# Kernel optimization log

Hardware: AMD Instinct MI355X
Metric: run time of the kernel (lower is better)

## Reference

```python
import jax, jax.numpy as jnp
import numpy as np

B, T, S0 = 8, 4, 4096
D_MODEL, H, D, R, RANK = 2048, 16, 128, 64, 512
C = D - R  # content dim = 64


def _rope(x, positions):
    # x: [B, H, T, R]; rotate-half style RoPE as in the torch module
    half = x.shape[-1] // 2
    inv_freq = 1.0 / (10000.0 ** (jnp.arange(half, dtype=jnp.float32) / half))
    freqs = positions.astype(jnp.float32)[:, None] * inv_freq[None, :]  # [T, half]
    cos = jnp.cos(freqs)[None, None].astype(x.dtype)
    sin = jnp.sin(freqs)[None, None].astype(x.dtype)
    x1, x2 = x[..., :half], x[..., half:]
    return jnp.concatenate([x1 * cos - x2 * sin, x1 * sin + x2 * cos], axis=-1)


def setup_inputs() -> dict:
    key = jax.random.key(0)
    ks = jax.random.split(key, 9)
    s = 0.02
    return {
        "x": jax.random.normal(ks[0], (B, T, D_MODEL), jnp.float32),
        "cache_c_kv": jax.random.normal(ks[1], (B, S0, RANK), jnp.float32),
        "cache_k_rope": jax.random.normal(ks[2], (B, S0, H, R), jnp.float32),
        "w_q": jax.random.normal(ks[3], (D_MODEL, H * C), jnp.float32) * s,
        "w_q_rope": jax.random.normal(ks[4], (D_MODEL, H * R), jnp.float32) * s,
        "w_kv_down": jax.random.normal(ks[5], (D_MODEL, RANK), jnp.float32) * s,
        "w_kv_up": jax.random.normal(ks[6], (RANK, H * D), jnp.float32) * s,
        "w_k_rope": jax.random.normal(ks[7], (D_MODEL, H * R), jnp.float32) * s,
        "w_out": jax.random.normal(ks[8], (H * D, D_MODEL), jnp.float32) * s,
    }


def reference(x, cache_c_kv, cache_k_rope, w_q, w_q_rope, w_kv_down, w_kv_up, w_k_rope, w_out):
    cache_len = cache_c_kv.shape[1]
    positions = jnp.arange(cache_len, cache_len + T)

    # queries
    q_content = (x @ w_q).reshape(B, T, H, C).transpose(0, 2, 1, 3)        # [B,H,T,C]
    q_rope = (x @ w_q_rope).reshape(B, T, H, R).transpose(0, 2, 1, 3)      # [B,H,T,R]
    q_rope = _rope(q_rope, positions)
    q = jnp.concatenate([q_content, q_rope], axis=-1)                       # [B,H,T,D]

    # new compressed kv + rope keys, append to cache
    c_kv_new = x @ w_kv_down                                                # [B,T,RANK]
    k_rope_new = (x @ w_k_rope).reshape(B, T, H, R).transpose(0, 2, 1, 3)
    k_rope_new = _rope(k_rope_new, positions).transpose(0, 2, 1, 3)         # [B,T,H,R]
    c_kv = jnp.concatenate([cache_c_kv, c_kv_new], axis=1)                  # [B,S,RANK]
    k_rope = jnp.concatenate([cache_k_rope, k_rope_new], axis=1)            # [B,S,H,R]

    # decompress full cache every step (the expensive MLA pattern)
    S = c_kv.shape[1]
    kv = (c_kv @ w_kv_up).reshape(B, S, H, D)                               # [B,S,H,D]
    k_content = kv[..., :C].transpose(0, 2, 1, 3)                           # [B,H,S,C]
    v = kv.transpose(0, 2, 1, 3)                                            # [B,H,S,D]
    k = jnp.concatenate([k_content, k_rope.transpose(0, 2, 1, 3)], axis=-1) # [B,H,S,D]

    # kv_cache present => is_prefill False => no causal mask (faithful to source)
    scale = 1.0 / jnp.sqrt(jnp.asarray(D, dtype=q.dtype))
    scores = jnp.einsum('bhtd,bhsd->bhts', q, k) * scale
    attn = jax.nn.softmax(scores, axis=-1)
    out = jnp.einsum('bhts,bhsd->bhtd', attn, v)                            # [B,H,T,D]
    out = out.transpose(0, 2, 1, 3).reshape(B, T, H * D)
    return out @ w_out                                                       # [B,T,D_MODEL]
```

## Files before the change

kernel.cpp:

```cpp
#include <hip/hip_runtime.h>
#include <hip/hip_fp16.h>
#include <cmath>

#define BB 8
#define TT 4
#define HH 16
#define DDIM 128
#define RRDIM 64
#define CCDIM 64
#define RANKC 512
#define DMODEL 2048
#define S0C 4096
#define NQ 64
#define HD 2048
#define NACT 3584
#define NSC 65
#define NG 17
#define SPAD 4160
#define SCALE_ATT 0.08838834764831845f

typedef __attribute__((ext_vector_type(8))) short bf16x8;
typedef __attribute__((ext_vector_type(4))) float f32x4;
typedef unsigned short ushortT;

#define AIDX(row, kk) ((row)*132 + (((row)>>2)<<2) + (kk))

static __device__ __forceinline__ unsigned short f2bf(float x) {
  unsigned u = __float_as_uint(x);
  u += 0x7FFFu + ((u >> 16) & 1u);
  return (unsigned short)(u >> 16);
}
static __device__ __forceinline__ unsigned pk2(float a, float b) {
  return (unsigned)f2bf(a) | ((unsigned)f2bf(b) << 16);
}

__global__ __launch_bounds__(256) void k_front(const float* __restrict__ A,
                                               const float* __restrict__ w0,
                                               const float* __restrict__ w1,
                                               const float* __restrict__ w2,
                                               const float* __restrict__ w3,
                                               const float* __restrict__ cckv,
                                               float* __restrict__ part,
                                               ushortT* __restrict__ ckvB,
                                               ushortT* __restrict__ ckvT) {
  __shared__ float shf[4352];
  const int tid = threadIdx.x;
  const int bx = blockIdx.x;
  if (bx < 448) {
    const int cb = bx % 28;
    const int k0 = (bx / 28) * 128;
    const float* W; int N, lc0, off;
    if (cb < 8)       { W = w0; N = 1024; lc0 = cb * 128;        off = 0; }
    else if (cb < 16) { W = w1; N = 1024; lc0 = (cb - 8) * 128;  off = 1024; }
    else if (cb < 20) { W = w2; N = 512;  lc0 = (cb - 16) * 128; off = 2048; }
    else              { W = w3; N = 1024; lc0 = (cb - 20) * 128; off = 2560; }
    {
      const int row = tid >> 3;
      const int kseg = (tid & 7) * 16;
      const float4* s4 = reinterpret_cast<const float4*>(A + (size_t)row * DMODEL + k0 + kseg);
      float4 v0 = s4[0], v1 = s4[1], v2 = s4[2], v3 = s4[3];
      *reinterpret_cast<float4*>(&shf[AIDX(row, kseg)])      = v0;
      *reinterpret_cast<float4*>(&shf[AIDX(row, kseg + 4)])  = v1;
      *reinterpret_cast<float4*>(&shf[AIDX(row, kseg + 8)])  = v2;
      *reinterpret_cast<float4*>(&shf[AIDX(row, kseg + 12)]) = v3;
    }
    __syncthreads();
    const int cg = tid & 31;
    const int rg = tid >> 5;
    float acc[4][4];
    #pragma unroll
    for (int r = 0; r < 4; ++r)
      #pragma unroll
      for (int c = 0; c < 4; ++c) acc[r][c] = 0.f;
    #pragma unroll 4
    for (int kk = 0; kk < 128; ++kk) {
      const float4 w4 = *reinterpret_cast<const float4*>(W + (size_t)(k0 + kk) * N + lc0 + cg * 4);
      const float wv[4] = {w4.x, w4.y, w4.z, w4.w};
      #pragma unroll
      for (int r = 0; r < 4; ++r) {
        const float av = shf[AIDX(rg * 4 + r, kk)];
        #pragma unroll
        for (int c = 0; c < 4; ++c) acc[r][c] = fmaf(av, wv[c], acc[r][c]);
      }
    }
    #pragma unroll
    for (int r = 0; r < 4; ++r) {
      float4 o = make_float4(acc[r][0], acc[r][1], acc[r][2], acc[r][3]);
      *reinterpret_cast<float4*>(part + ((size_t)(bx / 28) * 32 + rg * 4 + r) * NACT + off + lc0 + cg * 4) = o;
    }
  } else if (bx < 960) {
    ushortT* tlds = reinterpret_cast<ushortT*>(shf);
    const int idx = bx - 448;
    const int b = idx >> 6, c = idx & 63;
    const float* src = cckv + ((size_t)b * S0C + c * 64) * RANKC;
    ushortT* dstB = ckvB + ((size_t)(b * NSC + c) * 64) * RANKC;
    ushortT* dstT = ckvT + ((size_t)(b * NSC + c) * RANKC) * 64;
    const int s = tid >> 2, rq = tid & 3;
    const int rloc = tid >> 1, shalf = (tid & 1) * 32;
    for (int slab = 0; slab < 4; ++slab) {
      const int r0 = slab * 128;
      #pragma unroll
      for (int i = 0; i < 8; ++i) {
        const float4 v = *reinterpret_cast<const float4*>(src + (size_t)s * RANKC + r0 + rq * 32 + i * 4);
        const uint2 pk = make_uint2(pk2(v.x, v.y), pk2(v.z, v.w));
        *reinterpret_cast<uint2*>(&tlds[s * 136 + rq * 32 + i * 4]) = pk;
        *reinterpret_cast<uint2*>(&dstB[(size_t)s * RANKC + r0 + rq * 32 + i * 4]) = pk;
      }
      __syncthreads();
      unsigned pkv[16];
      #pragma unroll
      for (int k = 0; k < 16; ++k) {
        const unsigned t0 = tlds[(shalf + 2 * k)     * 136 + rloc];
        const unsigned t1 = tlds[(shalf + 2 * k + 1) * 136 + rloc];
        pkv[k] = t0 | (t1 << 16);
      }
      uint4* d = reinterpret_cast<uint4*>(dstT + ((size_t)(r0 + rloc)) * 64 + shalf);
      d[0] = make_uint4(pkv[0], pkv[1], pkv[2], pkv[3]);
      d[1] = make_uint4(pkv[4], pkv[5], pkv[6], pkv[7]);
      d[2] = make_uint4(pkv[8], pkv[9], pkv[10], pkv[11]);
      d[3] = make_uint4(pkv[12], pkv[13], pkv[14], pkv[15]);
      __syncthreads();
    }
  } else if (bx < 968) {
    const int b = bx - 960;
    uint4* p = reinterpret_cast<uint4*>(ckvB + ((size_t)(b * NSC + 64) * 64) * RANKC);
    const uint4 z = make_uint4(0, 0, 0, 0);
    for (int i = tid; i < 4096; i += 256) p[i] = z;
  } else {
    const int b = bx - 968;
    uint4* p = reinterpret_cast<uint4*>(ckvT + ((size_t)(b * NSC + 64) * RANKC) * 64);
    const uint4 z = make_uint4(0, 0, 0, 0);
    for (int i = tid; i < 4096; i += 256) p[i] = z;
  }
}

__global__ __launch_bounds__(256) void k_proj(const float* __restrict__ A,
                                              const float* __restrict__ W,
                                              float* __restrict__ part,
                                              int N, int NTOT, int coloff) {
  __shared__ float a_lds[4352];
  const int tid = threadIdx.x;
  const int c0 = blockIdx.x * 128;
  const int k0 = blockIdx.y * 128;
  {
    const int row = tid >> 3;
    const int kseg = (tid & 7) * 16;
    const float4* s4 = reinterpret_cast<const float4*>(A + (size_t)row * DMODEL + k0 + kseg);
    float4 v0 = s4[0], v1 = s4[1], v2 = s4[2], v3 = s4[3];
    *reinterpret_cast<float4*>(&a_lds[AIDX(row, kseg)])      = v0;
    *reinterpret_cast<float4*>(&a_lds[AIDX(row, kseg + 4)])  = v1;
    *reinterpret_cast<float4*>(&a_lds[AIDX(row, kseg + 8)])  = v2;
    *reinterpret_cast<float4*>(&a_lds[AIDX(row, kseg + 12)]) = v3;
  }
  __syncthreads();
  const int cg = tid & 31;
  const int rg = tid >> 5;
  float acc[4][4];
  #pragma unroll
  for (int r = 0; r < 4; ++r)
    #pragma unroll
    for (int c = 0; c < 4; ++c) acc[r][c] = 0.f;
  #pragma unroll 4
  for (int kk = 0; kk < 128; ++kk) {
    const float4 w4 = *reinterpret_cast<const float4*>(W + (size_t)(k0 + kk) * N + c0 + cg * 4);
    const float wv[4] = {w4.x, w4.y, w4.z, w4.w};
    #pragma unroll
    for (int r = 0; r < 4; ++r) {
      const float av = a_lds[AIDX(rg * 4 + r, kk)];
      #pragma unroll
      for (int c = 0; c < 4; ++c) acc[r][c] = fmaf(av, wv[c], acc[r][c]);
    }
  }
  #pragma unroll
  for (int r = 0; r < 4; ++r) {
    float4 o = make_float4(acc[r][0], acc[r][1], acc[r][2], acc[r][3]);
    *reinterpret_cast<float4*>(part + ((size_t)blockIdx.y * 32 + rg * 4 + r) * NTOT + coloff + c0 + cg * 4) = o;
  }
}

__global__ __launch_bounds__(256) void k_reduce(const float* __restrict__ part,
                                                float* __restrict__ out, int total, int nsplit) {
  int g = blockIdx.x * 256 + threadIdx.x;
  if (g >= total) return;
  float s = 0.f;
  #pragma unroll 4
  for (int c = 0; c < nsplit; ++c) s += part[(size_t)c * total + g];
  out[g] = s;
}

__global__ __launch_bounds__(256) void k_qlatrope(const float* __restrict__ act,
                                                  const float* __restrict__ wup,
                                                  ushortT* __restrict__ qlat,
                                                  float* __restrict__ qrope,
                                                  float* __restrict__ krn,
                                                  ushortT* __restrict__ ckvB,
                                                  ushortT* __restrict__ ckvT) {
  __shared__ float wt[64 * 132];
  __shared__ float a_s[32 * 68];
  const int tid = threadIdx.x;
  const int bx = blockIdx.x;
  if (bx < 64) {
    const int h = bx & 15;
    const int r0 = (bx >> 4) * 128;
    {
      const int r = tid >> 1;
      const int cseg = (tid & 1) * 32;
      const float* src = wup + (size_t)(r0 + r) * HD + h * DDIM + cseg;
      #pragma unroll
      for (int u = 0; u < 8; ++u) {
        const float4 v = *reinterpret_cast<const float4*>(src + u * 4);
        wt[(cseg + u * 4 + 0) * 132 + r] = v.x;
        wt[(cseg + u * 4 + 1) * 132 + r] = v.y;
        wt[(cseg + u * 4 + 2) * 132 + r] = v.z;
        wt[(cseg + u * 4 + 3) * 132 + r] = v.w;
      }
    }
    {
      const int bt = tid >> 3;
      const int cseg = (tid & 7) * 8;
      const float4* s4 = reinterpret_cast<const float4*>(act + (size_t)bt * NACT + h * CCDIM + cseg);
      float4 v0 = s4[0], v1 = s4[1];
      *reinterpret_cast<float4*>(&a_s[bt * 68 + cseg])     = v0;
      *reinterpret_cast<float4*>(&a_s[bt * 68 + cseg + 4]) = v1;
    }
    __syncthreads();
    const int r = tid & 127;
    const int bth = tid >> 7;
    float acc[16];
    #pragma unroll
    for (int i = 0; i < 16; ++i) acc[i] = 0.f;
    #pragma unroll 8
    for (int c = 0; c < 64; ++c) {
      const float wv = wt[c * 132 + r];
      #pragma unroll
      for (int i = 0; i < 16; ++i)
        acc[i] = fmaf(a_s[(bth * 16 + i) * 68 + c], wv, acc[i]);
    }
    #pragma unroll
    for (int i = 0; i < 16; ++i) {
      const int bt = bth * 16 + i;
      const int b = bt >> 2, t = bt & 3;
      qlat[((size_t)(b * NQ) + h * TT + t) * RANKC + r0 + r] = f2bf(acc[i]);
    }
    return;
  }
  int g = (bx - 64) * 256 + tid;
  if (g < BB * TT * HH * 32) {
    const int hj = g & 31;
    const int h = (g >> 5) & 15;
    const int t = (g >> 9) & 3;
    const int b = g >> 11;
    const float* arow = act + (size_t)(b * TT + t) * NACT + 1024 + h * RRDIM;
    const float x1 = arow[hj], x2 = arow[hj + 32];
    const double fr = (double)(S0C + t) * pow(10000.0, -(double)hj / 32.0);
    const float cs = (float)cos(fr), sn = (float)sin(fr);
    const int qi = h * TT + t;
    qrope[((size_t)b * NQ + qi) * RRDIM + hj]      = x1 * cs - x2 * sn;
    qrope[((size_t)b * NQ + qi) * RRDIM + hj + 32] = x1 * sn + x2 * cs;
    return;
  }
  g -= BB * TT * HH * 32;
  if (g < BB * TT * HH * 32) {
    const int hj = g & 31;
    const int h = (g >> 5) & 15;
    const int t = (g >> 9) & 3;
    const int b = g >> 11;
    const float* arow = act + (size_t)(b * TT + t) * NACT + 2560 + h * RRDIM;
    const float x1 = arow[hj], x2 = arow[hj + 32];
    const double fr = (double)(S0C + t) * pow(10000.0, -(double)hj / 32.0);
    const float cs = (float)cos(fr), sn = (float)sin(fr);
    krn[((size_t)(b * TT + t) * HH + h) * RRDIM + hj]      = x1 * cs - x2 * sn;
    krn[((size_t)(b * TT + t) * HH + h) * RRDIM + hj + 32] = x1 * sn + x2 * cs;
    return;
  }
  g -= BB * TT * HH * 32;
  if (g < BB * TT * RANKC) {
    const int r = g & 511;
    const int bt = g >> 9;
    const int b = bt >> 2, t = bt & 3;
    const ushortT bv = f2bf(act[(size_t)bt * NACT + 2048 + r]);
    ckvB[(((size_t)(b * NSC + 64) * 64) + t) * RANKC + r] = bv;
    ckvT[(((size_t)(b * NSC + 64) * RANKC) + r) * 64 + t] = bv;
  }
}

__global__ __launch_bounds__(256) void k_rscore(const float* __restrict__ cache_kr,
                                                const float* __restrict__ krn,
                                                const float* __restrict__ qrope,
                                                __half* __restrict__ rs) {
  const int bh = blockIdx.x;
  const int b = bh >> 4, h = bh & 15;
  const int tid = threadIdx.x;
  const int ql = tid & 3;
  float4 qf[4][4];
  const float* qrb = qrope + ((size_t)b * NQ + h * TT) * RRDIM;
  #pragma unroll
  for (int t = 0; t < 4; ++t)
    #pragma unroll
    for (int u = 0; u < 4; ++u)
      qf[t][u] = *reinterpret_cast<const float4*>(qrb + t * RRDIM + ql * 16 + u * 4);
  const int s0 = blockIdx.y * 512;
  #pragma unroll 1
  for (int pass = 0; pass < 8; ++pass) {
    const int s = s0 + pass * 64 + (tid >> 2);
    if (s < 4100) {
      const float* krow = (s < S0C)
        ? cache_kr + (((size_t)b * S0C + s) * HH + h) * RRDIM
        : krn + (((size_t)b * TT + (s - S0C)) * HH + h) * RRDIM;
      float p[4] = {0.f, 0.f, 0.f, 0.f};
      #pragma unroll
      for (int u = 0; u < 4; ++u) {
        const float4 kv = *reinterpret_cast<const float4*>(krow + ql * 16 + u * 4);
        #pragma unroll
        for (int t = 0; t < 4; ++t) {
          p[t] += kv.x * qf[t][u].x + kv.y * qf[t][u].y
                + kv.z * qf[t][u].z + kv.w * qf[t][u].w;
        }
      }
      #pragma unroll
      for (int t = 0; t < 4; ++t) {
        p[t] += __shfl_xor(p[t], 1, 4);
        p[t] += __shfl_xor(p[t], 2, 4);
      }
      rs[((size_t)bh * 4 + ql) * SPAD + s] = __float2half(p[ql] * SCALE_ATT);
    }
  }
}

__global__ __launch_bounds__(128) void k_score(
    const ushortT* __restrict__ ckvB, const ushortT* __restrict__ qlat,
    const __half* __restrict__ rs, float* __restrict__ ml,
    ushortT* __restrict__ Pg) {
  __shared__ ushortT PL[2][16 * 72];
  const int tid = threadIdx.x;
  const int wv = tid >> 6;
  const int lane = tid & 63;
  const int lm = lane & 15, lg = lane >> 4;
  const int b = blockIdx.x, chunk = blockIdx.y;
  const int qbase = blockIdx.z * 32 + wv * 16;
  const int scnt = (chunk < 64) ? 64 : TT;

  const ushortT* qrow = qlat + ((size_t)b * NQ + qbase + lm) * RANKC + lg * 8;
  bf16x8 qa[16];
  #pragma unroll
  for (int ks = 0; ks < 16; ++ks)
    qa[ks] = *reinterpret_cast<const bf16x8*>(qrow + ks * 32);

  const ushortT* bbase = ckvB + ((size_t)(b * NSC + chunk) * 64) * RANKC;
  f32x4 acc[4];
  #pragma unroll
  for (int st = 0; st < 4; ++st) acc[st] = (f32x4){0.f, 0.f, 0.f, 0.f};
  #pragma unroll
  for (int ks = 0; ks < 16; ++ks) {
    #pragma unroll
    for (int st = 0; st < 4; ++st) {
      const bf16x8 bf = *reinterpret_cast<const bf16x8*>(
          bbase + (size_t)(st * 16 + lm) * RANKC + ks * 32 + lg * 8);
      acc[st] = __builtin_amdgcn_mfma_f32_16x16x32_bf16(qa[ks], bf, acc[st], 0, 0, 0);
    }
  }

  #pragma unroll
  for (int reg = 0; reg < 4; ++reg) {
    const int qi = qbase + lg * 4 + reg;
    const __half* rp = rs + (((size_t)(b * HH) + (qi >> 2)) * TT + (qi & 3)) * SPAD + chunk * 64;
    float vvv[4];
    float mx = -1e30f;
    #pragma unroll
    for (int st = 0; st < 4; ++st) {
      const int sl = st * 16 + lm;
      const float val = (sl < scnt)
          ? fmaf(acc[st][reg], SCALE_ATT, __half2float(rp[sl]))
          : -1e30f;
      vvv[st] = val;
      mx = fmaxf(mx, val);
    }
    #pragma unroll
    for (int off = 1; off < 16; off <<= 1) mx = fmaxf(mx, __shfl_xor(mx, off, 16));
    float sum = 0.f;
    #pragma unroll
    for (int st = 0; st < 4; ++st) {
      const float p = __expf(vvv[st] - mx);
      vvv[st] = p;
      sum += p;
    }
    #pragma unroll
    for (int off = 1; off < 16; off <<= 1) sum += __shfl_xor(sum, off, 16);
    #pragma unroll
    for (int st = 0; st < 4; ++st)
      PL[wv][(lg * 4 + reg) * 72 + st * 16 + lm] = f2bf(vvv[st]);
    if (lm == 0) {
      const size_t mb = (((size_t)b * NSC + chunk) * NQ + qi) * 2;
      ml[mb] = mx; ml[mb + 1] = sum;
    }
  }
  __syncthreads();
  {
    const int row = lane >> 2, seg = (lane & 3) * 16;
    const uint4* sp = reinterpret_cast<const uint4*>(&PL[wv][row * 72 + seg]);
    uint4* dp = reinterpret_cast<uint4*>(
        Pg + ((size_t)(b * NSC + chunk) * NQ + qbase + row) * 64 + seg);
    dp[0] = sp[0]; dp[1] = sp[1];
  }
}

__global__ __launch_bounds__(128) void k_pv(
    const ushortT* __restrict__ ckvT, const ushortT* __restrict__ Pg,
    const float* __restrict__ ml, float* __restrict__ olat,
    float* __restrict__ mlg) {
  const int tid = threadIdx.x;
  const int wv = tid >> 6;
  const int lane = tid & 63;
  const int lm = lane & 15, lg = lane >> 4;
  const int b = blockIdx.x, g = blockIdx.y;
  const int rg = blockIdx.z >> 1, qh = blockIdx.z & 1;
  const int qbase = qh * 32 + wv * 16;
  const int nc = (g < 16) ? 4 : 1;
  const int c0 = (g < 16) ? g * 4 : 64;

  float m_cl = -1e30f, l_cl = 0.f;
  if (lg < nc) {
    const size_t mb = (((size_t)b * NSC + c0 + lg) * NQ + qbase + lm) * 2;
    m_cl = ml[mb]; l_cl = ml[mb + 1];
  }
  float mg = fmaxf(m_cl, __shfl_xor(m_cl, 16));
  mg = fmaxf(mg, __shfl_xor(mg, 32));
  const float wgt = (lg < nc) ? __expf(m_cl - mg) : 0.f;
  float la = l_cl * wgt;
  la += __shfl_xor(la, 16);
  la += __shfl_xor(la, 32);
  if (rg == 0 && lg == 0) {
    const size_t gb = (((size_t)b * NG + g) * NQ + qbase + lm) * 2;
    mlg[gb] = mg; mlg[gb + 1] = la;
  }
  float wf[4][4];
  #pragma unroll
  for (int c = 0; c < 4; ++c)
    #pragma unroll
    for (int reg = 0; reg < 4; ++reg)
      wf[c][reg] = __shfl(wgt, c * 16 + lg * 4 + reg);

  f32x4 OACC[8];
  #pragma unroll
  for (int nt = 0; nt < 8; ++nt) OACC[nt] = (f32x4){0.f, 0.f, 0.f, 0.f};

  for (int c = 0; c < nc; ++c) {
    const ushortT* pb = Pg + ((size_t)(b * NSC + c0 + c) * NQ + qbase + lm) * 64 + lg * 8;
    const bf16x8 pa0 = *reinterpret_cast<const bf16x8*>(pb);
    const bf16x8 pa1 = *reinterpret_cast<const bf16x8*>(pb + 32);
    const ushortT* vb = ckvT + (((size_t)(b * NSC + c0 + c) * RANKC) + rg * 128 + lm) * 64 + lg * 8;
    f32x4 a2[8];
    #pragma unroll
    for (int nt = 0; nt < 8; ++nt) a2[nt] = (f32x4){0.f, 0.f, 0.f, 0.f};
    #pragma unroll
    for (int nt = 0; nt < 8; ++nt) {
      const bf16x8 b0 = *reinterpret_cast<const bf16x8*>(vb + (size_t)nt * 16 * 64);
      const bf16x8 b1 = *reinterpret_cast<const bf16x8*>(vb + (size_t)nt * 16 * 64 + 32);
      a2[nt] = __builtin_amdgcn_mfma_f32_16x16x32_bf16(pa0, b0, a2[nt], 0, 0, 0);
      a2[nt] = __builtin_amdgcn_mfma_f32_16x16x32_bf16(pa1, b1, a2[nt], 0, 0, 0);
    }
    const f32x4 wv4 = {wf[c][0], wf[c][1], wf[c][2], wf[c][3]};
    #pragma unroll
    for (int nt = 0; nt < 8; ++nt) OACC[nt] += wv4 * a2[nt];
  }

  const size_t obase = ((size_t)(b * NG + g) * NQ) * RANKC;
  #pragma unroll
  for (int nt = 0; nt < 8; ++nt)
    #pragma unroll
    for (int reg = 0; reg < 4; ++reg)
      olat[obase + (size_t)(qbase + lg * 4 + reg) * RANKC + rg * 128 + nt * 16 + lm] = OACC[nt][reg];
}

__global__ __launch_bounds__(512) void k_combF(const float* __restrict__ mlg,
                                               const float* __restrict__ olat,
                                               const float* __restrict__ wup,
                                               float* __restrict__ ohead) {
  __shared__ float wrow[4][20];
  __shared__ float att_lds[4][516];
  const int h = blockIdx.x, b = blockIdx.y;
  const int tid = threadIdx.x;
  const int wave = tid >> 6;
  const int i = wave >> 1;
  const int rhalf = wave & 1;
  const int rl = tid & 63;
  const int qi = h * TT + i;
  float m1 = -1e30f, l1 = 0.f;
  if (rl < NG) {
    const size_t base = (((size_t)b * NG + rl) * NQ + qi) * 2;
    m1 = mlg[base]; l1 = mlg[base + 1];
  }
  float M = m1;
  #pragma unroll
  for (int off = 1; off < 64; off <<= 1) M = fmaxf(M, __shfl_xor(M, off));
  float L = (rl < NG) ? l1 * __expf(m1 - M) : 0.f;
  #pragma unroll
  for (int off = 1; off < 64; off <<= 1) L += __shfl_xor(L, off);
  const float invL = 1.0f / L;
  if (rl < NG) wrow[i][rl] = __expf(m1 - M) * invL;
  __syncthreads();
  const int r0 = rhalf * 256 + rl * 4;
  float o0 = 0.f, o1 = 0.f, o2 = 0.f, o3 = 0.f;
  for (int c = 0; c < NG; ++c) {
    const float w = wrow[i][c];
    const float4 v = *reinterpret_cast<const float4*>(
        olat + (((size_t)b * NG + c) * NQ + qi) * RANKC + r0);
    o0 = fmaf(v.x, w, o0); o1 = fmaf(v.y, w, o1);
    o2 = fmaf(v.z, w, o2); o3 = fmaf(v.w, w, o3);
  }
  *reinterpret_cast<float4*>(&att_lds[i][r0]) = make_float4(o0, o1, o2, o3);
  __syncthreads();
  const int col = tid & 127;
  const int t = tid >> 7;
  float acc = 0.f;
  #pragma unroll 8
  for (int r = 0; r < RANKC; ++r)
    acc = fmaf(att_lds[t][r], wup[(size_t)r * HD + h * DDIM + col], acc);
  ohead[(size_t)(b * TT + t) * HD + h * DDIM + col] = acc;
}

extern "C" void kernel_launch(void* const* d_in, const int* in_sizes, int n_in,
                              void* d_out, int out_size, void* d_ws, size_t ws_size,
                              hipStream_t stream) {
  const float* x     = (const float*)d_in[0];
  const float* cckv  = (const float*)d_in[1];
  const float* ckr   = (const float*)d_in[2];
  const float* w_q   = (const float*)d_in[3];
  const float* w_qr  = (const float*)d_in[4];
  const float* w_kvd = (const float*)d_in[5];
  const float* w_kvu = (const float*)d_in[6];
  const float* w_kr  = (const float*)d_in[7];
  const float* w_out = (const float*)d_in[8];
  float* out = (float*)d_out;
  float* ws = (float*)d_ws;

  size_t off = 0;
  float* act      = ws + off; off += 32ull * NACT;
  ushortT* qlat   = (ushortT*)(ws + off); off += 131072;
  float* qrope    = ws + off; off += 32768;
  float* krn      = ws + off; off += 32768;
  float* mlb      = ws + off; off += (size_t)BB * NSC * NQ * 2;
  float* mlgb     = ws + off; off += (size_t)BB * NG * NQ * 2;
  float* ohead    = ws + off; off += 65536;
  __half* rsb     = (__half*)(ws + off); off += 1064960;
  ushortT* ckvB   = (ushortT*)(ws + off); off += 8519680;
  ushortT* ckvT   = (ushortT*)(ws + off); off += 8519680;
  ushortT* Pgb    = (ushortT*)(ws + off); off += 1064960;
  float* regB  = ws + off;
  float* part0 = regB;
  float* olat  = regB;
  float* part3 = regB;

  k_front<<<dim3(976), 256, 0, stream>>>(x, w_q, w_qr, w_kvd, w_kr, cckv, part0, ckvB, ckvT);
  k_reduce<<<dim3(448), 256, 0, stream>>>(part0, act, 32 * NACT, 16);
  k_qlatrope<<<dim3(256), 256, 0, stream>>>(act, w_kvu, qlat, qrope, krn, ckvB, ckvT);
  k_rscore<<<dim3(128, 9), 256, 0, stream>>>(ckr, krn, qrope, rsb);

  k_score<<<dim3(BB, NSC, 2), 128, 0, stream>>>(ckvB, qlat, rsb, mlb, Pgb);
  k_pv<<<dim3(BB, NG, 8), 128, 0, stream>>>(ckvT, Pgb, mlb, olat, mlgb);

  k_combF<<<dim3(16, 8), 512, 0, stream>>>(mlgb, olat, w_kvu, ohead);
  k_proj<<<dim3(16, 16), 256, 0, stream>>>(ohead, w_out, part3, 2048, 2048, 0);
  k_reduce<<<dim3(256), 256, 0, stream>>>(part3, out, 32 * HD, 16);
}
```

Baseline: 213.0 us.

## Fuse reduce, q-latent, rope-score stages and drop bf16 row-major cache copy

Three kernels (the split-K reduce, the q-latent/rope kernel and the rope-score kernel) are merged into a single k_mid kernel that sums the split-K partials directly where each stage needs them. The row-major bf16 copy of the compressed cache is removed. k_score now reads the fp32 cache and converts it to bf16 on the fly, with new tokens held in a small fp32 buffer. The score and PV kernels use 256-thread blocks covering all 64 queries, which halves their grid sizes. This cuts launches and a large bf16 write, but the score kernel reads twice as many bytes per cache element and repeats the partial sums per block.

```diff
diff --git a/kernel.cpp b/kernel.cpp
--- a/kernel.cpp
+++ b/kernel.cpp
@@ -33,6 +33,11 @@
 static __device__ __forceinline__ unsigned pk2(float a, float b) {
   return (unsigned)f2bf(a) | ((unsigned)f2bf(b) << 16);
 }
+static __device__ __forceinline__ bf16x8 cvt8(const float4 a, const float4 b) {
+  union { uint4 u; bf16x8 h; } r;
+  r.u = make_uint4(pk2(a.x, a.y), pk2(a.z, a.w), pk2(b.x, b.y), pk2(b.z, b.w));
+  return r.h;
+}
 
 __global__ __launch_bounds__(256) void k_front(const float* __restrict__ A,
                                                const float* __restrict__ w0,
@@ -41,8 +46,8 @@
                                                const float* __restrict__ w3,
                                                const float* __restrict__ cckv,
                                                float* __restrict__ part,
-                                               ushortT* __restrict__ ckvB,
-                                               ushortT* __restrict__ ckvT) {
+                                               ushortT* __restrict__ ckvT,
+                                               float* __restrict__ ckvn) {
   __shared__ float shf[4352];
   const int tid = threadIdx.x;
   const int bx = blockIdx.x;
@@ -93,7 +98,6 @@
     const int idx = bx - 448;
     const int b = idx >> 6, c = idx & 63;
     const float* src = cckv + ((size_t)b * S0C + c * 64) * RANKC;
-    ushortT* dstB = ckvB + ((size_t)(b * NSC + c) * 64) * RANKC;
     ushortT* dstT = ckvT + ((size_t)(b * NSC + c) * RANKC) * 64;
     const int s = tid >> 2, rq = tid & 3;
     const int rloc = tid >> 1, shalf = (tid & 1) * 32;
@@ -102,9 +106,8 @@
       #pragma unroll
       for (int i = 0; i < 8; ++i) {
         const float4 v = *reinterpret_cast<const float4*>(src + (size_t)s * RANKC + r0 + rq * 32 + i * 4);
-        const uint2 pk = make_uint2(pk2(v.x, v.y), pk2(v.z, v.w));
-        *reinterpret_cast<uint2*>(&tlds[s * 136 + rq * 32 + i * 4]) = pk;
-        *reinterpret_cast<uint2*>(&dstB[(size_t)s * RANKC + r0 + rq * 32 + i * 4]) = pk;
+        *reinterpret_cast<uint2*>(&tlds[s * 136 + rq * 32 + i * 4]) =
+            make_uint2(pk2(v.x, v.y), pk2(v.z, v.w));
       }
       __syncthreads();
       unsigned pkv[16];
@@ -121,17 +124,362 @@
       d[3] = make_uint4(pkv[12], pkv[13], pkv[14], pkv[15]);
       __syncthreads();
     }
-  } else if (bx < 968) {
+  } else {
     const int b = bx - 960;
-    uint4* p = reinterpret_cast<uint4*>(ckvB + ((size_t)(b * NSC + 64) * 64) * RANKC);
     const uint4 z = make_uint4(0, 0, 0, 0);
+    uint4* p = reinterpret_cast<uint4*>(ckvT + ((size_t)(b * NSC + 64) * RANKC) * 64);
     for (int i = tid; i < 4096; i += 256) p[i] = z;
+    uint4* q = reinterpret_cast<uint4*>(ckvn + ((size_t)b * 64 + 4) * RANKC);
+    for (int i = tid; i < 7680; i += 256) q[i] = z;
+  }
+}
+
+__global__ __launch_bounds__(256) void k_mid(const float* __restrict__ part0,
+                                             const float* __restrict__ cache_kr,
+                                             const float* __restrict__ wup,
+                                             ushortT* __restrict__ qlat,
+                                             float* __restrict__ ckvn,
+                                             ushortT* __restrict__ ckvT,
+                                             __half* __restrict__ rs) {
+  __shared__ float smid[10880];
+  const int tid = threadIdx.x;
+  const int bx = blockIdx.x;
+  if (bx < 1152) {
+    const int bh = bx / 9, sy = bx % 9;
+    const int b = bh >> 4, h = bh & 15;
+    float* raw_q = smid;
+    float* raw_k = smid + 256;
+    float* qr_l  = smid + 512;
+    float* kr_l  = smid + 768;
+    {
+      const int t = tid >> 6, j = tid & 63;
+      const size_t rowoff = (size_t)(b * TT + t) * NACT;
+      float sq = 0.f, sk = 0.f;
+      #pragma unroll 4
+      for (int ks = 0; ks < 16; ++ks) {
+        const float* pp = part0 + (size_t)ks * (32 * NACT) + rowoff;
+        sq += pp[1024 + h * 64 + j];
+        sk += pp[2560 + h * 64 + j];
+      }
+      raw_q[t * 64 + j] = sq;
+      raw_k[t * 64 + j] = sk;
+    }
+    __syncthreads();
+    {
+      const int t = tid >> 6, j = tid & 63;
+      const int j2 = j & 31;
+      const double inv = pow(10000.0, -(double)j2 / 32.0);
+      const double fr = (double)(S0C + t) * inv;
+      const float cs = (float)cos(fr), sn = (float)sin(fr);
+      const float qa = raw_q[t * 64 + j], qp = raw_q[t * 64 + (j ^ 32)];
+      const float ka = raw_k[t * 64 + j], kp = raw_k[t * 64 + (j ^ 32)];
+      float qv, kv;
+      if (j < 32) { qv = qa * cs - qp * sn; kv = ka * cs - kp * sn; }
+      else        { qv = qp * sn + qa * cs; kv = kp * sn + ka * cs; }
+      qr_l[t * 64 + j] = qv * SCALE_ATT;
+      kr_l[t * 64 + j] = kv;
+    }
+    __syncthreads();
+    const int ql = tid & 3;
+    float4 qf[4][4];
+    #pragma unroll
+    for (int t = 0; t < 4; ++t)
+      #pragma unroll
+      for (int u = 0; u < 4; ++u)
+        qf[t][u] = *reinterpret_cast<const float4*>(&qr_l[t * 64 + ql * 16 + u * 4]);
+    const int s0 = sy * 512;
+    #pragma unroll 1
+    for (int pass = 0; pass < 8; ++pass) {
+      const int s = s0 + pass * 64 + (tid >> 2);
+      if (s < 4100) {
+        float p[4] = {0.f, 0.f, 0.f, 0.f};
+        if (s < S0C) {
+          const float* krow = cache_kr + (((size_t)b * S0C + s) * HH + h) * RRDIM;
+          #pragma unroll
+          for (int u = 0; u < 4; ++u) {
+            const float4 kv = *reinterpret_cast<const float4*>(krow + ql * 16 + u * 4);
+            #pragma unroll
+            for (int t = 0; t < 4; ++t)
+              p[t] += kv.x * qf[t][u].x + kv.y * qf[t][u].y
+                    + kv.z * qf[t][u].z + kv.w * qf[t][u].w;
+          }
+        } else {
+          const float* krow = &kr_l[(s - S0C) * 64];
+          #pragma unroll
+          for (int u = 0; u < 4; ++u) {
+            const float4 kv = *reinterpret_cast<const float4*>(krow + ql * 16 + u * 4);
+            #pragma unroll
+            for (int t = 0; t < 4; ++t)
+              p[t] += kv.x * qf[t][u].x + kv.y * qf[t][u].y
+                    + kv.z * qf[t][u].z + kv.w * qf[t][u].w;
+          }
+        }
+        #pragma unroll
+        for (int t = 0; t < 4; ++t) {
+          p[t] += __shfl_xor(p[t], 1, 4);
+          p[t] += __shfl_xor(p[t], 2, 4);
+        }
+        rs[((size_t)bh * 4 + ql) * SPAD + s] = __float2half(p[ql]);
+      }
+    }
+  } else if (bx < 1216) {
+    const int lx = bx - 1152;
+    const int h = lx & 15;
+    const int r0 = (lx >> 4) * 128;
+    float* wt  = smid;
+    float* a_s = smid + 8448;
+    {
+      const int r = tid >> 1;
+      const int cseg = (tid & 1) * 32;
+      const float* src = wup + (size_t)(r0 + r) * HD + h * DDIM + cseg;
+      #pragma unroll
+      for (int u = 0; u < 8; ++u) {
+        const float4 v = *reinterpret_cast<const float4*>(src + u * 4);
+        wt[(cseg + u * 4 + 0) * 132 + r] = v.x;
+        wt[(cseg + u * 4 + 1) * 132 + r] = v.y;
+        wt[(cseg + u * 4 + 2) * 132 + r] = v.z;
+        wt[(cseg + u * 4 + 3) * 132 + r] = v.w;
+      }
+    }
+    {
+      const int bt = tid >> 3;
+      const int c8 = (tid & 7) * 8;
+      float v[8] = {0.f,0.f,0.f,0.f,0.f,0.f,0.f,0.f};
+      #pragma unroll 4
+      for (int ks = 0; ks < 16; ++ks) {
+        const float4* pp = reinterpret_cast<const float4*>(
+            part0 + (size_t)ks * (32 * NACT) + (size_t)bt * NACT + h * CCDIM + c8);
+        const float4 x0 = pp[0], x1 = pp[1];
+        v[0]+=x0.x; v[1]+=x0.y; v[2]+=x0.z; v[3]+=x0.w;
+        v[4]+=x1.x; v[5]+=x1.y; v[6]+=x1.z; v[7]+=x1.w;
+      }
+      #pragma unroll
+      for (int u = 0; u < 8; ++u) a_s[bt * 68 + c8 + u] = v[u];
+    }
+    __syncthreads();
+    const int r = tid & 127;
+    const int bth = tid >> 7;
+    float acc[16];
+    #pragma unroll
+    for (int i = 0; i < 16; ++i) acc[i] = 0.f;
+    #pragma unroll 8
+    for (int c = 0; c < 64; ++c) {
+      const float wv = wt[c * 132 + r];
+      #pragma unroll
+      for (int i = 0; i < 16; ++i)
+        acc[i] = fmaf(a_s[(bth * 16 + i) * 68 + c], wv, acc[i]);
+    }
+    #pragma unroll
+    for (int i = 0; i < 16; ++i) {
+      const int bt = bth * 16 + i;
+      const int b = bt >> 2, t = bt & 3;
+      qlat[((size_t)(b * NQ) + h * TT + t) * RANKC + r0 + r] = f2bf(acc[i]);
+    }
   } else {
-    const int b = bx - 968;
-    uint4* p = reinterpret_cast<uint4*>(ckvT + ((size_t)(b * NSC + 64) * RANKC) * 64);
-    const uint4 z = make_uint4(0, 0, 0, 0);
-    for (int i = tid; i < 4096; i += 256) p[i] = z;
-  }
+    const int g = (bx - 1216) * 256 + tid;
+    const int r = g & 511;
+    const int bt = g >> 9;
+    const int b = bt >> 2, t = bt & 3;
+    float s = 0.f;
+    #pragma unroll 4
+    for (int ks = 0; ks < 16; ++ks)
+      s += part0[(size_t)ks * (32 * NACT) + (size_t)bt * NACT + 2048 + r];
+    ckvn[((size_t)b * 64 + t) * RANKC + r] = s;
+    ckvT[(((size_t)(b * NSC + 64) * RANKC) + r) * 64 + t] = f2bf(s);
+  }
+}
+
+__global__ __launch_bounds__(256) void k_score(
+    const float* __restrict__ cckv, const float* __restrict__ ckvn,
+    const ushortT* __restrict__ qlat, const __half* __restrict__ rs,
+    float* __restrict__ ml, ushortT* __restrict__ Pg) {
+  __shared__ ushortT PL[64 * 72];
+  const int tid = threadIdx.x;
+  const int wv = tid >> 6;
+  const int lane = tid & 63;
+  const int lm = lane & 15, lg = lane >> 4;
+  const int b = blockIdx.x, chunk = blockIdx.y;
+  const int qbase = wv * 16;
+  const int scnt = (chunk < 64) ? 64 : TT;
+  const float* bsrc = (chunk < 64)
+      ? cckv + ((size_t)b * S0C + (size_t)chunk * 64) * RANKC
+      : ckvn + (size_t)b * 64 * RANKC;
+
+  const ushortT* qrow = qlat + ((size_t)b * NQ + qbase + lm) * RANKC + lg * 8;
+  bf16x8 qa[16];
+  #pragma unroll
+  for (int ks = 0; ks < 16; ++ks)
+    qa[ks] = *reinterpret_cast<const bf16x8*>(qrow + ks * 32);
+
+  f32x4 acc[4];
+  #pragma unroll
+  for (int st = 0; st < 4; ++st) acc[st] = (f32x4){0.f, 0.f, 0.f, 0.f};
+  #pragma unroll
+  for (int ks = 0; ks < 16; ++ks) {
+    #pragma unroll
+    for (int st = 0; st < 4; ++st) {
+      const float4* bp = reinterpret_cast<const float4*>(
+          bsrc + (size_t)(st * 16 + lm) * RANKC + ks * 32 + lg * 8);
+      acc[st] = __builtin_amdgcn_mfma_f32_16x16x32_bf16(qa[ks], cvt8(bp[0], bp[1]), acc[st], 0, 0, 0);
+    }
+  }
+
+  #pragma unroll
+  for (int reg = 0; reg < 4; ++reg) {
+    const int qi = qbase + lg * 4 + reg;
+    const __half* rp = rs + (((size_t)(b * HH) + (qi >> 2)) * TT + (qi & 3)) * SPAD + chunk * 64;
+    float vvv[4];
+    float mx = -1e30f;
+    #pragma unroll
+    for (int st = 0; st < 4; ++st) {
+      const int sl = st * 16 + lm;
+      const float val = (sl < scnt)
+          ? fmaf(acc[st][reg], SCALE_ATT, __half2float(rp[sl]))
+          : -1e30f;
+      vvv[st] = val;
+      mx = fmaxf(mx, val);
+    }
+    #pragma unroll
+    for (int off = 1; off < 16; off <<= 1) mx = fmaxf(mx, __shfl_xor(mx, off, 16));
+    float sum = 0.f;
+    #pragma unroll
+    for (int st = 0; st < 4; ++st) {
+      const float p = __expf(vvv[st] - mx);
+      vvv[st] = p;
+      sum += p;
+    }
+    #pragma unroll
+    for (int off = 1; off < 16; off <<= 1) sum += __shfl_xor(sum, off, 16);
+    #pragma unroll
+    for (int st = 0; st < 4; ++st)
+      PL[(qbase + lg * 4 + reg) * 72 + st * 16 + lm] = f2bf(vvv[st]);
+    if (lm == 0) {
+      const size_t mb = (((size_t)b * NSC + chunk) * NQ + qi) * 2;
+      ml[mb] = mx; ml[mb + 1] = sum;
+    }
+  }
+  __syncthreads();
+  {
+    const int row = tid >> 2, seg = (tid & 3) * 16;
+    const uint4* sp = reinterpret_cast<const uint4*>(&PL[row * 72 + seg]);
+    uint4* dp = reinterpret_cast<uint4*>(
+        Pg + ((size_t)(b * NSC + chunk) * NQ + row) * 64 + seg);
+    dp[0] = sp[0]; dp[1] = sp[1];
+  }
+}
+
+__global__ __launch_bounds__(256) void k_pv(
+    const ushortT* __restrict__ ckvT, const ushortT* __restrict__ Pg,
+    const float* __restrict__ ml, float* __restrict__ olat,
+    float* __restrict__ mlg) {
+  const int tid = threadIdx.x;
+  const int wv = tid >> 6;
+  const int lane = tid & 63;
+  const int lm = lane & 15, lg = lane >> 4;
+  const int b = blockIdx.x, g = blockIdx.y, rg = blockIdx.z;
+  const int qbase = wv * 16;
+  const int nc = (g < 16) ? 4 : 1;
+  const int c0 = (g < 16) ? g * 4 : 64;
+
+  float m_cl = -1e30f, l_cl = 0.f;
+  if (lg < nc) {
+    const size_t mb = (((size_t)b * NSC + c0 + lg) * NQ + qbase + lm) * 2;
+    m_cl = ml[mb]; l_cl = ml[mb + 1];
+  }
+  float mg = fmaxf(m_cl, __shfl_xor(m_cl, 16));
+  mg = fmaxf(mg, __shfl_xor(mg, 32));
+  const float wgt = (lg < nc) ? __expf(m_cl - mg) : 0.f;
+  float la = l_cl * wgt;
+  la += __shfl_xor(la, 16);
+  la += __shfl_xor(la, 32);
+  if (rg == 0 && lg == 0) {
+    const size_t gb = (((size_t)b * NG + g) * NQ + qbase + lm) * 2;
+    mlg[gb] = mg; mlg[gb + 1] = la;
+  }
+  float wf[4][4];
+  #pragma unroll
+  for (int c = 0; c < 4; ++c)
+    #pragma unroll
+    for (int reg = 0; reg < 4; ++reg)
+      wf[c][reg] = __shfl(wgt, c * 16 + lg * 4 + reg);
+
+  f32x4 OACC[8];
+  #pragma unroll
+  for (int nt = 0; nt < 8; ++nt) OACC[nt] = (f32x4){0.f, 0.f, 0.f, 0.f};
+
+  for (int c = 0; c < nc; ++c) {
+    const ushortT* pb = Pg + ((size_t)(b * NSC + c0 + c) * NQ + qbase + lm) * 64 + lg * 8;
+    const bf16x8 pa0 = *reinterpret_cast<const bf16x8*>(pb);
+    const bf16x8 pa1 = *reinterpret_cast<const bf16x8*>(pb + 32);
+    const ushortT* vb = ckvT + (((size_t)(b * NSC + c0 + c) * RANKC) + rg * 128 + lm) * 64 + lg * 8;
+    f32x4 a2[8];
+    #pragma unroll
+    for (int nt = 0; nt < 8; ++nt) a2[nt] = (f32x4){0.f, 0.f, 0.f, 0.f};
+    #pragma unroll
+    for (int nt = 0; nt < 8; ++nt) {
+      const bf16x8 b0 = *reinterpret_cast<const bf16x8*>(vb + (size_t)nt * 16 * 64);
+      const bf16x8 b1 = *reinterpret_cast<const bf16x8*>(vb + (size_t)nt * 16 * 64 + 32);
+      a2[nt] = __builtin_amdgcn_mfma_f32_16x16x32_bf16(pa0, b0, a2[nt], 0, 0, 0);
+      a2[nt] = __builtin_amdgcn_mfma_f32_16x16x32_bf16(pa1, b1, a2[nt], 0, 0, 0);
+    }
+    const f32x4 wv4 = {wf[c][0], wf[c][1], wf[c][2], wf[c][3]};
+    #pragma unroll
+    for (int nt = 0; nt < 8; ++nt) OACC[nt] += wv4 * a2[nt];
+  }
+
+  const size_t obase = ((size_t)(b * NG + g) * NQ) * RANKC;
+  #pragma unroll
+  for (int nt = 0; nt < 8; ++nt)
+    #pragma unroll
+    for (int reg = 0; reg < 4; ++reg)
+      olat[obase + (size_t)(qbase + lg * 4 + reg) * RANKC + rg * 128 + nt * 16 + lm] = OACC[nt][reg];
+}
+
+__global__ __launch_bounds__(512) void k_combF(const float* __restrict__ mlg,
+                                               const float* __restrict__ olat,
+                                               const float* __restrict__ wup,
+                                               float* __restrict__ ohead) {
+  __shared__ float wrow[4][20];
+  __shared__ float att_lds[4][516];
+  const int h = blockIdx.x, b = blockIdx.y;
+  const int tid = threadIdx.x;
+  const int wave = tid >> 6;
+  const int i = wave >> 1;
+  const int rhalf = wave & 1;
+  const int rl = tid & 63;
+  const int qi = h * TT + i;
+  float m1 = -1e30f, l1 = 0.f;
+  if (rl < NG) {
+    const size_t base = (((size_t)b * NG + rl) * NQ + qi) * 2;
+    m1 = mlg[base]; l1 = mlg[base + 1];
+  }
+  float M = m1;
+  #pragma unroll
+  for (int off = 1; off < 64; off <<= 1) M = fmaxf(M, __shfl_xor(M, off));
+  float L = (rl < NG) ? l1 * __expf(m1 - M) : 0.f;
+  #pragma unroll
+  for (int off = 1; off < 64; off <<= 1) L += __shfl_xor(L, off);
+  const float invL = 1.0f / L;
+  if (rl < NG) wrow[i][rl] = __expf(m1 - M) * invL;
+  __syncthreads();
+  const int r0 = rhalf * 256 + rl * 4;
+  float o0 = 0.f, o1 = 0.f, o2 = 0.f, o3 = 0.f;
+  for (int c = 0; c < NG; ++c) {
+    const float w = wrow[i][c];
+    const float4 v = *reinterpret_cast<const float4*>(
+        olat + (((size_t)b * NG + c) * NQ + qi) * RANKC + r0);
+    o0 = fmaf(v.x, w, o0); o1 = fmaf(v.y, w, o1);
+    o2 = fmaf(v.z, w, o2); o3 = fmaf(v.w, w, o3);
+  }
+  *reinterpret_cast<float4*>(&att_lds[i][r0]) = make_float4(o0, o1, o2, o3);
+  __syncthreads();
+  const int col = tid & 127;
+  const int t = tid >> 7;
+  float acc = 0.f;
+  #pragma unroll 8
+  for (int r = 0; r < RANKC; ++r)
+    acc = fmaf(att_lds[t][r], wup[(size_t)r * HD + h * DDIM + col], acc);
+  ohead[(size_t)(b * TT + t) * HD + h * DDIM + col] = acc;
 }
 
 __global__ __launch_bounds__(256) void k_proj(const float* __restrict__ A,
@@ -188,337 +536,6 @@
   out[g] = s;
 }
 
-__global__ __launch_bounds__(256) void k_qlatrope(const float* __restrict__ act,
-                                                  const float* __restrict__ wup,
-                                                  ushortT* __restrict__ qlat,
-                                                  float* __restrict__ qrope,
-                                                  float* __restrict__ krn,
-                                                  ushortT* __restrict__ ckvB,
-                                                  ushortT* __restrict__ ckvT) {
-  __shared__ float wt[64 * 132];
-  __shared__ float a_s[32 * 68];
-  const int tid = threadIdx.x;
-  const int bx = blockIdx.x;
-  if (bx < 64) {
-    const int h = bx & 15;
-    const int r0 = (bx >> 4) * 128;
-    {
-      const int r = tid >> 1;
-      const int cseg = (tid & 1) * 32;
-      const float* src = wup + (size_t)(r0 + r) * HD + h * DDIM + cseg;
-      #pragma unroll
-      for (int u = 0; u < 8; ++u) {
-        const float4 v = *reinterpret_cast<const float4*>(src + u * 4);
-        wt[(cseg + u * 4 + 0) * 132 + r] = v.x;
-        wt[(cseg + u * 4 + 1) * 132 + r] = v.y;
-        wt[(cseg + u * 4 + 2) * 132 + r] = v.z;
-        wt[(cseg + u * 4 + 3) * 132 + r] = v.w;
-      }
-    }
-    {
-      const int bt = tid >> 3;
-      const int cseg = (tid & 7) * 8;
-      const float4* s4 = reinterpret_cast<const float4*>(act + (size_t)bt * NACT + h * CCDIM + cseg);
-      float4 v0 = s4[0], v1 = s4[1];
-      *reinterpret_cast<float4*>(&a_s[bt * 68 + cseg])     = v0;
-      *reinterpret_cast<float4*>(&a_s[bt * 68 + cseg + 4]) = v1;
-    }
-    __syncthreads();
-    const int r = tid & 127;
-    const int bth = tid >> 7;
-    float acc[16];
-    #pragma unroll
-    for (int i = 0; i < 16; ++i) acc[i] = 0.f;
-    #pragma unroll 8
-    for (int c = 0; c < 64; ++c) {
-      const float wv = wt[c * 132 + r];
-      #pragma unroll
-      for (int i = 0; i < 16; ++i)
-        acc[i] = fmaf(a_s[(bth * 16 + i) * 68 + c], wv, acc[i]);
-    }
-    #pragma unroll
-    for (int i = 0; i < 16; ++i) {
-      const int bt = bth * 16 + i;
-      const int b = bt >> 2, t = bt & 3;
-      qlat[((size_t)(b * NQ) + h * TT + t) * RANKC + r0 + r] = f2bf(acc[i]);
-    }
-    return;
-  }
-  int g = (bx - 64) * 256 + tid;
-  if (g < BB * TT * HH * 32) {
-    const int hj = g & 31;
-    const int h = (g >> 5) & 15;
-    const int t = (g >> 9) & 3;
-    const int b = g >> 11;
-    const float* arow = act + (size_t)(b * TT + t) * NACT + 1024 + h * RRDIM;
-    const float x1 = arow[hj], x2 = arow[hj + 32];
-    const double fr = (double)(S0C + t) * pow(10000.0, -(double)hj / 32.0);
-    const float cs = (float)cos(fr), sn = (float)sin(fr);
-    const int qi = h * TT + t;
-    qrope[((size_t)b * NQ + qi) * RRDIM + hj]      = x1 * cs - x2 * sn;
-    qrope[((size_t)b * NQ + qi) * RRDIM + hj + 32] = x1 * sn + x2 * cs;
-    return;
-  }
-  g -= BB * TT * HH * 32;
-  if (g < BB * TT * HH * 32) {
-    const int hj = g & 31;
-    const int h = (g >> 5) & 15;
-    const int t = (g >> 9) & 3;
-    const int b = g >> 11;
-    const float* arow = act + (size_t)(b * TT + t) * NACT + 2560 + h * RRDIM;
-    const float x1 = arow[hj], x2 = arow[hj + 32];
-    const double fr = (double)(S0C + t) * pow(10000.0, -(double)hj / 32.0);
-    const float cs = (float)cos(fr), sn = (float)sin(fr);
-    krn[((size_t)(b * TT + t) * HH + h) * RRDIM + hj]      = x1 * cs - x2 * sn;
-    krn[((size_t)(b * TT + t) * HH + h) * RRDIM + hj + 32] = x1 * sn + x2 * cs;
-    return;
-  }
-  g -= BB * TT * HH * 32;
-  if (g < BB * TT * RANKC) {
-    const int r = g & 511;
-    const int bt = g >> 9;
-    const int b = bt >> 2, t = bt & 3;
-    const ushortT bv = f2bf(act[(size_t)bt * NACT + 2048 + r]);
-    ckvB[(((size_t)(b * NSC + 64) * 64) + t) * RANKC + r] = bv;
-    ckvT[(((size_t)(b * NSC + 64) * RANKC) + r) * 64 + t] = bv;
-  }
-}
-
-__global__ __launch_bounds__(256) void k_rscore(const float* __restrict__ cache_kr,
-                                                const float* __restrict__ krn,
-                                                const float* __restrict__ qrope,
-                                                __half* __restrict__ rs) {
-  const int bh = blockIdx.x;
-  const int b = bh >> 4, h = bh & 15;
-  const int tid = threadIdx.x;
-  const int ql = tid & 3;
-  float4 qf[4][4];
-  const float* qrb = qrope + ((size_t)b * NQ + h * TT) * RRDIM;
-  #pragma unroll
-  for (int t = 0; t < 4; ++t)
-    #pragma unroll
-    for (int u = 0; u < 4; ++u)
-      qf[t][u] = *reinterpret_cast<const float4*>(qrb + t * RRDIM + ql * 16 + u * 4);
-  const int s0 = blockIdx.y * 512;
-  #pragma unroll 1
-  for (int pass = 0; pass < 8; ++pass) {
-    const int s = s0 + pass * 64 + (tid >> 2);
-    if (s < 4100) {
-      const float* krow = (s < S0C)
-        ? cache_kr + (((size_t)b * S0C + s) * HH + h) * RRDIM
-        : krn + (((size_t)b * TT + (s - S0C)) * HH + h) * RRDIM;
-      float p[4] = {0.f, 0.f, 0.f, 0.f};
-      #pragma unroll
-      for (int u = 0; u < 4; ++u) {
-        const float4 kv = *reinterpret_cast<const float4*>(krow + ql * 16 + u * 4);
-        #pragma unroll
-        for (int t = 0; t < 4; ++t) {
-          p[t] += kv.x * qf[t][u].x + kv.y * qf[t][u].y
-                + kv.z * qf[t][u].z + kv.w * qf[t][u].w;
-        }
-      }
-      #pragma unroll
-      for (int t = 0; t < 4; ++t) {
-        p[t] += __shfl_xor(p[t], 1, 4);
-        p[t] += __shfl_xor(p[t], 2, 4);
-      }
-      rs[((size_t)bh * 4 + ql) * SPAD + s] = __float2half(p[ql] * SCALE_ATT);
-    }
-  }
-}
-
-__global__ __launch_bounds__(128) void k_score(
-    const ushortT* __restrict__ ckvB, const ushortT* __restrict__ qlat,
-    const __half* __restrict__ rs, float* __restrict__ ml,
-    ushortT* __restrict__ Pg) {
-  __shared__ ushortT PL[2][16 * 72];
-  const int tid = threadIdx.x;
-  const int wv = tid >> 6;
-  const int lane = tid & 63;
-  const int lm = lane & 15, lg = lane >> 4;
-  const int b = blockIdx.x, chunk = blockIdx.y;
-  const int qbase = blockIdx.z * 32 + wv * 16;
-  const int scnt = (chunk < 64) ? 64 : TT;
-
-  const ushortT* qrow = qlat + ((size_t)b * NQ + qbase + lm) * RANKC + lg * 8;
-  bf16x8 qa[16];
-  #pragma unroll
-  for (int ks = 0; ks < 16; ++ks)
-    qa[ks] = *reinterpret_cast<const bf16x8*>(qrow + ks * 32);
-
-  const ushortT* bbase = ckvB + ((size_t)(b * NSC + chunk) * 64) * RANKC;
-  f32x4 acc[4];
-  #pragma unroll
-  for (int st = 0; st < 4; ++st) acc[st] = (f32x4){0.f, 0.f, 0.f, 0.f};
-  #pragma unroll
-  for (int ks = 0; ks < 16; ++ks) {
-    #pragma unroll
-    for (int st = 0; st < 4; ++st) {
-      const bf16x8 bf = *reinterpret_cast<const bf16x8*>(
-          bbase + (size_t)(st * 16 + lm) * RANKC + ks * 32 + lg * 8);
-      acc[st] = __builtin_amdgcn_mfma_f32_16x16x32_bf16(qa[ks], bf, acc[st], 0, 0, 0);
-    }
-  }
-
-  #pragma unroll
-  for (int reg = 0; reg < 4; ++reg) {
-    const int qi = qbase + lg * 4 + reg;
-    const __half* rp = rs + (((size_t)(b * HH) + (qi >> 2)) * TT + (qi & 3)) * SPAD + chunk * 64;
-    float vvv[4];
-    float mx = -1e30f;
-    #pragma unroll
-    for (int st = 0; st < 4; ++st) {
-      const int sl = st * 16 + lm;
-      const float val = (sl < scnt)
-          ? fmaf(acc[st][reg], SCALE_ATT, __half2float(rp[sl]))
-          : -1e30f;
-      vvv[st] = val;
-      mx = fmaxf(mx, val);
-    }
-    #pragma unroll
-    for (int off = 1; off < 16; off <<= 1) mx = fmaxf(mx, __shfl_xor(mx, off, 16));
-    float sum = 0.f;
-    #pragma unroll
-    for (int st = 0; st < 4; ++st) {
-      const float p = __expf(vvv[st] - mx);
-      vvv[st] = p;
-      sum += p;
-    }
-    #pragma unroll
-    for (int off = 1; off < 16; off <<= 1) sum += __shfl_xor(sum, off, 16);
-    #pragma unroll
-    for (int st = 0; st < 4; ++st)
-      PL[wv][(lg * 4 + reg) * 72 + st * 16 + lm] = f2bf(vvv[st]);
-    if (lm == 0) {
-      const size_t mb = (((size_t)b * NSC + chunk) * NQ + qi) * 2;
-      ml[mb] = mx; ml[mb + 1] = sum;
-    }
-  }
-  __syncthreads();
-  {
-    const int row = lane >> 2, seg = (lane & 3) * 16;
-    const uint4* sp = reinterpret_cast<const uint4*>(&PL[wv][row * 72 + seg]);
-    uint4* dp = reinterpret_cast<uint4*>(
-        Pg + ((size_t)(b * NSC + chunk) * NQ + qbase + row) * 64 + seg);
-    dp[0] = sp[0]; dp[1] = sp[1];
-  }
-}
-
-__global__ __launch_bounds__(128) void k_pv(
-    const ushortT* __restrict__ ckvT, const ushortT* __restrict__ Pg,
-    const float* __restrict__ ml, float* __restrict__ olat,
-    float* __restrict__ mlg) {
-  const int tid = threadIdx.x;
-  const int wv = tid >> 6;
-  const int lane = tid & 63;
-  const int lm = lane & 15, lg = lane >> 4;
-  const int b = blockIdx.x, g = blockIdx.y;
-  const int rg = blockIdx.z >> 1, qh = blockIdx.z & 1;
-  const int qbase = qh * 32 + wv * 16;
-  const int nc = (g < 16) ? 4 : 1;
-  const int c0 = (g < 16) ? g * 4 : 64;
-
-  float m_cl = -1e30f, l_cl = 0.f;
-  if (lg < nc) {
-    const size_t mb = (((size_t)b * NSC + c0 + lg) * NQ + qbase + lm) * 2;
-    m_cl = ml[mb]; l_cl = ml[mb + 1];
-  }
-  float mg = fmaxf(m_cl, __shfl_xor(m_cl, 16));
-  mg = fmaxf(mg, __shfl_xor(mg, 32));
-  const float wgt = (lg < nc) ? __expf(m_cl - mg) : 0.f;
-  float la = l_cl * wgt;
-  la += __shfl_xor(la, 16);
-  la += __shfl_xor(la, 32);
-  if (rg == 0 && lg == 0) {
-    const size_t gb = (((size_t)b * NG + g) * NQ + qbase + lm) * 2;
-    mlg[gb] = mg; mlg[gb + 1] = la;
-  }
-  float wf[4][4];
-  #pragma unroll
-  for (int c = 0; c < 4; ++c)
-    #pragma unroll
-    for (int reg = 0; reg < 4; ++reg)
-      wf[c][reg] = __shfl(wgt, c * 16 + lg * 4 + reg);
-
-  f32x4 OACC[8];
-  #pragma unroll
-  for (int nt = 0; nt < 8; ++nt) OACC[nt] = (f32x4){0.f, 0.f, 0.f, 0.f};
-
-  for (int c = 0; c < nc; ++c) {
-    const ushortT* pb = Pg + ((size_t)(b * NSC + c0 + c) * NQ + qbase + lm) * 64 + lg * 8;
-    const bf16x8 pa0 = *reinterpret_cast<const bf16x8*>(pb);
-    const bf16x8 pa1 = *reinterpret_cast<const bf16x8*>(pb + 32);
-    const ushortT* vb = ckvT + (((size_t)(b * NSC + c0 + c) * RANKC) + rg * 128 + lm) * 64 + lg * 8;
-    f32x4 a2[8];
-    #pragma unroll
-    for (int nt = 0; nt < 8; ++nt) a2[nt] = (f32x4){0.f, 0.f, 0.f, 0.f};
-    #pragma unroll
-    for (int nt = 0; nt < 8; ++nt) {
-      const bf16x8 b0 = *reinterpret_cast<const bf16x8*>(vb + (size_t)nt * 16 * 64);
-      const bf16x8 b1 = *reinterpret_cast<const bf16x8*>(vb + (size_t)nt * 16 * 64 + 32);
-      a2[nt] = __builtin_amdgcn_mfma_f32_16x16x32_bf16(pa0, b0, a2[nt], 0, 0, 0);
-      a2[nt] = __builtin_amdgcn_mfma_f32_16x16x32_bf16(pa1, b1, a2[nt], 0, 0, 0);
-    }
-    const f32x4 wv4 = {wf[c][0], wf[c][1], wf[c][2], wf[c][3]};
-    #pragma unroll
-    for (int nt = 0; nt < 8; ++nt) OACC[nt] += wv4 * a2[nt];
-  }
-
-  const size_t obase = ((size_t)(b * NG + g) * NQ) * RANKC;
-  #pragma unroll
-  for (int nt = 0; nt < 8; ++nt)
-    #pragma unroll
-    for (int reg = 0; reg < 4; ++reg)
-      olat[obase + (size_t)(qbase + lg * 4 + reg) * RANKC + rg * 128 + nt * 16 + lm] = OACC[nt][reg];
-}
-
-__global__ __launch_bounds__(512) void k_combF(const float* __restrict__ mlg,
-                                               const float* __restrict__ olat,
-                                               const float* __restrict__ wup,
-                                               float* __restrict__ ohead) {
-  __shared__ float wrow[4][20];
-  __shared__ float att_lds[4][516];
-  const int h = blockIdx.x, b = blockIdx.y;
-  const int tid = threadIdx.x;
-  const int wave = tid >> 6;
-  const int i = wave >> 1;
-  const int rhalf = wave & 1;
-  const int rl = tid & 63;
-  const int qi = h * TT + i;
-  float m1 = -1e30f, l1 = 0.f;
-  if (rl < NG) {
-    const size_t base = (((size_t)b * NG + rl) * NQ + qi) * 2;
-    m1 = mlg[base]; l1 = mlg[base + 1];
-  }
-  float M = m1;
-  #pragma unroll
-  for (int off = 1; off < 64; off <<= 1) M = fmaxf(M, __shfl_xor(M, off));
-  float L = (rl < NG) ? l1 * __expf(m1 - M) : 0.f;
-  #pragma unroll
-  for (int off = 1; off < 64; off <<= 1) L += __shfl_xor(L, off);
-  const float invL = 1.0f / L;
-  if (rl < NG) wrow[i][rl] = __expf(m1 - M) * invL;
-  __syncthreads();
-  const int r0 = rhalf * 256 + rl * 4;
-  float o0 = 0.f, o1 = 0.f, o2 = 0.f, o3 = 0.f;
-  for (int c = 0; c < NG; ++c) {
-    const float w = wrow[i][c];
-    const float4 v = *reinterpret_cast<const float4*>(
-        olat + (((size_t)b * NG + c) * NQ + qi) * RANKC + r0);
-    o0 = fmaf(v.x, w, o0); o1 = fmaf(v.y, w, o1);
-    o2 = fmaf(v.z, w, o2); o3 = fmaf(v.w, w, o3);
-  }
-  *reinterpret_cast<float4*>(&att_lds[i][r0]) = make_float4(o0, o1, o2, o3);
-  __syncthreads();
-  const int col = tid & 127;
-  const int t = tid >> 7;
-  float acc = 0.f;
-  #pragma unroll 8
-  for (int r = 0; r < RANKC; ++r)
-    acc = fmaf(att_lds[t][r], wup[(size_t)r * HD + h * DDIM + col], acc);
-  ohead[(size_t)(b * TT + t) * HD + h * DDIM + col] = acc;
-}
-
 extern "C" void kernel_launch(void* const* d_in, const int* in_sizes, int n_in,
                               void* d_out, int out_size, void* d_ws, size_t ws_size,
                               hipStream_t stream) {
@@ -535,15 +552,12 @@
   float* ws = (float*)d_ws;
 
   size_t off = 0;
-  float* act      = ws + off; off += 32ull * NACT;
-  ushortT* qlat   = (ushortT*)(ws + off); off += 131072;
-  float* qrope    = ws + off; off += 32768;
-  float* krn      = ws + off; off += 32768;
+  ushortT* qlat   = (ushortT*)(ws + off); off += 65536;
+  float* ckvn     = ws + off; off += 262144;
   float* mlb      = ws + off; off += (size_t)BB * NSC * NQ * 2;
   float* mlgb     = ws + off; off += (size_t)BB * NG * NQ * 2;
   float* ohead    = ws + off; off += 65536;
   __half* rsb     = (__half*)(ws + off); off += 1064960;
-  ushortT* ckvB   = (ushortT*)(ws + off); off += 8519680;
   ushortT* ckvT   = (ushortT*)(ws + off); off += 8519680;
   ushortT* Pgb    = (ushortT*)(ws + off); off += 1064960;
   float* regB  = ws + off;
@@ -551,14 +565,10 @@
   float* olat  = regB;
   float* part3 = regB;
 
-  k_front<<<dim3(976), 256, 0, stream>>>(x, w_q, w_qr, w_kvd, w_kr, cckv, part0, ckvB, ckvT);
-  k_reduce<<<dim3(448), 256, 0, stream>>>(part0, act, 32 * NACT, 16);
-  k_qlatrope<<<dim3(256), 256, 0, stream>>>(act, w_kvu, qlat, qrope, krn, ckvB, ckvT);
-  k_rscore<<<dim3(128, 9), 256, 0, stream>>>(ckr, krn, qrope, rsb);
-
-  k_score<<<dim3(BB, NSC, 2), 128, 0, stream>>>(ckvB, qlat, rsb, mlb, Pgb);
-  k_pv<<<dim3(BB, NG, 8), 128, 0, stream>>>(ckvT, Pgb, mlb, olat, mlgb);
-
+  k_front<<<dim3(968), 256, 0, stream>>>(x, w_q, w_qr, w_kvd, w_kr, cckv, part0, ckvT, ckvn);
+  k_mid<<<dim3(1280), 256, 0, stream>>>(part0, ckr, w_kvu, qlat, ckvn, ckvT, rsb);
+  k_score<<<dim3(BB, NSC), 256, 0, stream>>>(cckv, ckvn, qlat, rsb, mlb, Pgb);
+  k_pv<<<dim3(BB, NG, 4), 256, 0, stream>>>(ckvT, Pgb, mlb, olat, mlgb);
   k_combF<<<dim3(16, 8), 512, 0, stream>>>(mlgb, olat, w_kvu, ohead);
   k_proj<<<dim3(16, 16), 256, 0, stream>>>(ohead, w_out, part3, 2048, 2048, 0);
   k_reduce<<<dim3(256), 256, 0, stream>>>(part3, out, 32 * HD, 16);
```

New measurement: 223.6 us. +5.0%, slower.
